# Performance work log

Hardware: AMD Instinct MI355X
Metric: run time of the kernel (lower is better)

Reference implementation:

```python
import jax, jax.numpy as jnp
import numpy as np
from jax.ops import segment_sum, segment_max

N, E = 50000, 800000
IN_FEATS, H, D_HID, N_CLASSES = 256, 4, 32, 47
NEG_SLOPE = 0.2


def leaky_relu(x, slope=NEG_SLOPE):
    return jnp.where(x >= 0, x, slope * x)


def gat_conv(h, W, attn_l, attn_r, src, dst, n_nodes, heads, d_out):
    # h: [N, F_in]; W: [F_in, heads*d_out]; attn_l/attn_r: [heads, d_out]
    feat = (h @ W).reshape(n_nodes, heads, d_out)          # [N, H, D]
    el = jnp.sum(feat * attn_l, axis=-1)                   # [N, H]
    er = jnp.sum(feat * attn_r, axis=-1)                   # [N, H]
    e = leaky_relu(el[src] + er[dst])                      # [E, H]
    # segment softmax over incoming edges of each dst node
    e_max = segment_max(e, dst, num_segments=n_nodes)      # [N, H]
    e_exp = jnp.exp(e - e_max[dst])                        # [E, H]
    denom = segment_sum(e_exp, dst, num_segments=n_nodes)  # [N, H]
    alpha = e_exp / denom[dst]                             # [E, H]
    msg = feat[src] * alpha[..., None]                     # [E, H, D]
    return segment_sum(msg, dst, num_segments=n_nodes)     # [N, H, D]


def setup_inputs() -> dict:
    key = jax.random.key(0)
    ks = jax.random.split(key, 12)
    hd = H * D_HID
    def glorot(k, shape):
        fan = shape[0] + shape[-1] if len(shape) == 2 else int(np.prod(shape))
        return jax.random.normal(k, shape, dtype=jnp.float32) * np.sqrt(2.0 / fan)
    return {
        "x": jax.random.normal(ks[0], (N, IN_FEATS), dtype=jnp.float32),
        "src": jax.random.randint(ks[1], (E,), 0, N),
        "dst": jax.random.randint(ks[2], (E,), 0, N),
        "W1": glorot(ks[3], (IN_FEATS, hd)),
        "al1": glorot(ks[4], (H, D_HID)),
        "ar1": glorot(ks[5], (H, D_HID)),
        "W2": glorot(ks[6], (hd, hd)),
        "al2": glorot(ks[7], (H, D_HID)),
        "ar2": glorot(ks[8], (H, D_HID)),
        "W3": glorot(ks[9], (hd, H * N_CLASSES)),
        "al3": glorot(ks[10], (H, N_CLASSES)),
        "ar3": glorot(ks[11], (H, N_CLASSES)),
    }


def reference(x, src, dst, W1, al1, ar1, W2, al2, ar2, W3, al3, ar3):
    # layer 1: ELU activation, flatten heads
    h = gat_conv(x, W1, al1, ar1, src, dst, N, H, D_HID)
    h = jax.nn.elu(h).reshape(N, H * D_HID)
    # layer 2
    h = gat_conv(h, W2, al2, ar2, src, dst, N, H, D_HID)
    h = jax.nn.elu(h).reshape(N, H * D_HID)
    # layer 3: no activation, mean over heads, log softmax
    h = gat_conv(h, W3, al3, ar3, src, dst, N, H, N_CLASSES)
    h = h.mean(axis=1)                                      # [N, n_classes]
    return jax.nn.log_softmax(h, axis=-1)
```

## Files before the change

kernel.cpp:

```cpp
#include <hip/hip_runtime.h>
#include <hip/hip_bf16.h>
#include <math.h>
#include <string.h>

#define N_NODES 50000
#define N_EDGES 800000
#define NH 4

typedef unsigned int u32;
typedef unsigned short u16;
typedef __attribute__((ext_vector_type(8))) short bf16x8;
typedef __attribute__((ext_vector_type(4))) float f32x4;

__device__ __forceinline__ u32 pack_bf2(float a, float b) {
    __hip_bfloat162 h2 = __float22bfloat162_rn(make_float2(a, b));
    u32 r;
    memcpy(&r, &h2, 4);
    return r;
}
__device__ __forceinline__ float2 bf2_to_f2(u32 u) {
    return make_float2(__uint_as_float(u << 16), __uint_as_float(u & 0xffff0000u));
}
__device__ __forceinline__ short bf16r(float f) {
    __hip_bfloat16 h = __float2bfloat16(f);
    short s;
    memcpy(&s, &h, 2);
    return s;
}

__device__ __forceinline__ float wred_max(float v) {
#pragma unroll
    for (int o = 32; o > 0; o >>= 1) v = fmaxf(v, __shfl_xor(v, o));
    return v;
}
__device__ __forceinline__ float wred_sum(float v) {
#pragma unroll
    for (int o = 32; o > 0; o >>= 1) v += __shfl_xor(v, o);
    return v;
}


__global__ void k_hist(const int* __restrict__ dst, int* __restrict__ deg) {
    int i = blockIdx.x * 256 + threadIdx.x;
    if (i < N_EDGES) atomicAdd(&deg[dst[i]], 1);
}

__global__ __launch_bounds__(1024) void k_scan1(const int* __restrict__ deg,
                                                int* __restrict__ offs,
                                                int* __restrict__ bsum) {
    __shared__ int tmp[1024];
    int b = blockIdx.x, t = threadIdx.x;
    int i = b * 1024 + t;
    int v = (i < N_NODES) ? deg[i] : 0;
    tmp[t] = v;
    __syncthreads();
    for (int off = 1; off < 1024; off <<= 1) {
        int add = (t >= off) ? tmp[t - off] : 0;
        __syncthreads();
        tmp[t] += add;
        __syncthreads();
    }
    if (i < N_NODES) offs[i] = tmp[t] - v;
    if (t == 1023) bsum[b] = tmp[t];
}

__global__ void k_scan2(int* __restrict__ bsum, int nb) {
    if (blockIdx.x == 0 && threadIdx.x == 0) {
        int run = 0;
        for (int b = 0; b < nb; ++b) { int v = bsum[b]; bsum[b] = run; run += v; }
    }
}

__global__ __launch_bounds__(1024) void k_scan3(int* __restrict__ offs,
                                                const int* __restrict__ bsum,
                                                int* __restrict__ cursor) {
    int b = blockIdx.x, t = threadIdx.x;
    int i = b * 1024 + t;
    if (i < N_NODES) {
        int o = offs[i] + bsum[b];
        offs[i] = o;
        cursor[i] = o;
    }
    if (b == 0 && t == 0) offs[N_NODES] = N_EDGES;
}

__global__ void k_scatter(const int* __restrict__ src, const int* __restrict__ dst,
                          int* __restrict__ cursor, int* __restrict__ csrc) {
    int i = blockIdx.x * 256 + threadIdx.x;
    if (i < N_EDGES) {
        int p = atomicAdd(&cursor[dst[i]], 1);
        csrc[p] = src[i];
    }
}

template <int K, int NOUT, int NP>
__global__ void prep_w(const float* __restrict__ W, u16* __restrict__ Wp) {
    constexpr int NT = NP / 16;
    int idx = blockIdx.x * 256 + threadIdx.x;
    int total = (K / 32) * NT * 64 * 8;
    if (idx >= total) return;
    int j = idx & 7;
    int lane = (idx >> 3) & 63;
    int rest = idx >> 9;
    int nt = rest % NT;
    int kt = rest / NT;
    int k = kt * 32 + (lane >> 4) * 8 + j;
    int col = nt * 16 + (lane & 15);
    float v = (col < NOUT) ? W[(size_t)k * NOUT + col] : 0.f;
    Wp[idx] = (u16)bf16r(v);
}

template <int K, int NOUT, int NP, bool AF32, bool DOTS>
__global__ __launch_bounds__(256) void gemm_mfma(const void* __restrict__ Av,
                                                 const u16* __restrict__ Wp,
                                                 u16* __restrict__ feat,
                                                 const float* __restrict__ al,
                                                 const float* __restrict__ ar,
                                                 float* __restrict__ el,
                                                 float* __restrict__ er) {
    constexpr int NT = NP / 16;
    constexpr int KT = K / 32;
    int w = threadIdx.x >> 6, l = threadIdx.x & 63;
    int tile_m0 = blockIdx.x * 64 + w * 16;
    int c15 = l & 15;
    int rowA = tile_m0 + c15;
    if (rowA >= N_NODES) rowA = N_NODES - 1;
    int g = l >> 4;

    f32x4 acc[NT];
#pragma unroll
    for (int nt = 0; nt < NT; ++nt) acc[nt] = (f32x4){0.f, 0.f, 0.f, 0.f};

    for (int kt = 0; kt < KT; ++kt) {
        bf16x8 a;
        if constexpr (AF32) {
            const float* ap = (const float*)Av + (size_t)rowA * K + kt * 32 + g * 8;
            float4 f0 = *reinterpret_cast<const float4*>(ap);
            float4 f1 = *reinterpret_cast<const float4*>(ap + 4);
            a[0] = bf16r(f0.x); a[1] = bf16r(f0.y); a[2] = bf16r(f0.z); a[3] = bf16r(f0.w);
            a[4] = bf16r(f1.x); a[5] = bf16r(f1.y); a[6] = bf16r(f1.z); a[7] = bf16r(f1.w);
        } else {
            a = *reinterpret_cast<const bf16x8*>((const u16*)Av + (size_t)rowA * K + kt * 32 + g * 8);
        }
        const u16* wp = Wp + ((size_t)kt * NT) * 512 + (size_t)l * 8;
#pragma unroll
        for (int nt = 0; nt < NT; ++nt) {
            bf16x8 b = *reinterpret_cast<const bf16x8*>(wp + nt * 512);
            acc[nt] = __builtin_amdgcn_mfma_f32_16x16x32_bf16(a, b, acc[nt], 0, 0, 0);
        }
    }

    int rowD0 = tile_m0 + g * 4;
#pragma unroll
    for (int nt = 0; nt < NT; ++nt) {
        int col = nt * 16 + c15;
#pragma unroll
        for (int r = 0; r < 4; ++r) {
            int row = rowD0 + r;
            if (row < N_NODES)
                feat[(size_t)row * NP + col] = (u16)bf16r(acc[nt][r]);
        }
    }

    if constexpr (DOTS) {
        float alv[NT], arv[NT];
#pragma unroll
        for (int nt = 0; nt < NT; ++nt) {
            alv[nt] = al[nt * 16 + c15];
            arv[nt] = ar[nt * 16 + c15];
        }
#pragma unroll
        for (int r = 0; r < 4; ++r) {
            float hlv[NH] = {0.f, 0.f, 0.f, 0.f};
            float hrv[NH] = {0.f, 0.f, 0.f, 0.f};
#pragma unroll
            for (int nt = 0; nt < NT; ++nt) {
                constexpr int NTH = NT / NH;
                int h = nt / NTH;
                hlv[h] = fmaf(acc[nt][r], alv[nt], hlv[h]);
                hrv[h] = fmaf(acc[nt][r], arv[nt], hrv[h]);
            }
#pragma unroll
            for (int o = 1; o < 16; o <<= 1) {
#pragma unroll
                for (int j = 0; j < NH; ++j) {
                    hlv[j] += __shfl_xor(hlv[j], o);
                    hrv[j] += __shfl_xor(hrv[j], o);
                }
            }
            int row = rowD0 + r;
            if (c15 == 0 && row < N_NODES) {
                *reinterpret_cast<float4*>(el + (size_t)row * NH) =
                    make_float4(hlv[0], hlv[1], hlv[2], hlv[3]);
                *reinterpret_cast<float4*>(er + (size_t)row * NH) =
                    make_float4(hrv[0], hrv[1], hrv[2], hrv[3]);
            }
        }
    }
}

template <int DH, int STRIDE>
__global__ __launch_bounds__(256) void attn_dots(const u16* __restrict__ feat,
                                                 const float* __restrict__ al,
                                                 const float* __restrict__ ar,
                                                 float* __restrict__ el,
                                                 float* __restrict__ er) {
    int wave = threadIdx.x >> 6, lane = threadIdx.x & 63;
    int n = blockIdx.x * 4 + wave;
    int h = lane >> 4, t = lane & 15;
    const u16* f = feat + (size_t)n * STRIDE + h * DH;
    const float* alh = al + h * DH;
    const float* arh = ar + h * DH;
    float sl = 0.f, sr = 0.f;
#pragma unroll
    for (int d0 = 0; d0 < DH; d0 += 16) {
        int d = d0 + t;
        if (d < DH) {
            float fv = __uint_as_float(((u32)f[d]) << 16);
            sl = fmaf(fv, alh[d], sl);
            sr = fmaf(fv, arh[d], sr);
        }
    }
#pragma unroll
    for (int o = 1; o < 16; o <<= 1) {
        sl += __shfl_xor(sl, o);
        sr += __shfl_xor(sr, o);
    }
    if (t == 0) { el[n * NH + h] = sl; er[n * NH + h] = sr; }
}

__device__ __forceinline__ int alpha_chunk(const float* __restrict__ el,
                                           const int* __restrict__ csrc,
                                           float4 erv, int base, int i1, int wave,
                                           float4 mref, float4 vinv, bool online,
                                           float (*lal)[64][4], int lane) {
    int e = base + lane;
    bool act = e < i1;
    int srcn = act ? csrc[e] : 0;
    float4 elv = make_float4(0.f, 0.f, 0.f, 0.f);
    if (act) elv = *reinterpret_cast<const float4*>(el + (size_t)srcn * NH);
    float e0 = elv.x + erv.x; e0 = e0 >= 0.f ? e0 : 0.2f * e0;
    float e1 = elv.y + erv.y; e1 = e1 >= 0.f ? e1 : 0.2f * e1;
    float e2 = elv.z + erv.z; e2 = e2 >= 0.f ? e2 : 0.2f * e2;
    float e3 = elv.w + erv.w; e3 = e3 >= 0.f ? e3 : 0.2f * e3;
    float4 a4;
    if (online) {
        const float NEG = -__builtin_inff();
        float f0 = act ? e0 : NEG, f1 = act ? e1 : NEG, f2 = act ? e2 : NEG, f3 = act ? e3 : NEG;
        float m0 = wred_max(f0), m1 = wred_max(f1), m2 = wred_max(f2), m3 = wred_max(f3);
        float p0 = act ? __expf(e0 - m0) : 0.f;
        float p1 = act ? __expf(e1 - m1) : 0.f;
        float p2 = act ? __expf(e2 - m2) : 0.f;
        float p3 = act ? __expf(e3 - m3) : 0.f;
        float s0 = wred_sum(p0), s1 = wred_sum(p1), s2 = wred_sum(p2), s3 = wred_sum(p3);
        a4 = make_float4(act ? p0 / s0 : 0.f, act ? p1 / s1 : 0.f,
                         act ? p2 / s2 : 0.f, act ? p3 / s3 : 0.f);
    } else {
        a4 = make_float4(act ? __expf(e0 - mref.x) * vinv.x : 0.f,
                         act ? __expf(e1 - mref.y) * vinv.y : 0.f,
                         act ? __expf(e2 - mref.z) * vinv.z : 0.f,
                         act ? __expf(e3 - mref.w) * vinv.w : 0.f);
    }
    *reinterpret_cast<float4*>(&lal[wave][lane][0]) = a4;
    return srcn;
}

__device__ __forceinline__ void stats_pass(const float* __restrict__ el,
                                           const int* __restrict__ csrc,
                                           float4 erv, int i0, int i1, int lane,
                                           float4& mout, float4& vout) {
    const float NEG = -__builtin_inff();
    float m0 = NEG, m1 = NEG, m2 = NEG, m3 = NEG;
    float s0 = 0.f, s1 = 0.f, s2 = 0.f, s3 = 0.f;
    for (int base = i0; base < i1; base += 64) {
        int i = base + lane;
        bool act = i < i1;
        int srcn = act ? csrc[i] : 0;
        float4 elv = make_float4(0.f, 0.f, 0.f, 0.f);
        if (act) elv = *reinterpret_cast<const float4*>(el + (size_t)srcn * NH);
        float e0 = elv.x + erv.x; e0 = e0 >= 0.f ? e0 : 0.2f * e0;
        float e1 = elv.y + erv.y; e1 = e1 >= 0.f ? e1 : 0.2f * e1;
        float e2 = elv.z + erv.z; e2 = e2 >= 0.f ? e2 : 0.2f * e2;
        float e3 = elv.w + erv.w; e3 = e3 >= 0.f ? e3 : 0.2f * e3;
        if (!act) { e0 = NEG; e1 = NEG; e2 = NEG; e3 = NEG; }
        float c0 = wred_max(e0), c1 = wred_max(e1), c2 = wred_max(e2), c3 = wred_max(e3);
        float nm0 = fmaxf(m0, c0), nm1 = fmaxf(m1, c1), nm2 = fmaxf(m2, c2), nm3 = fmaxf(m3, c3);
        float p0 = act ? __expf(e0 - nm0) : 0.f;
        float p1 = act ? __expf(e1 - nm1) : 0.f;
        float p2 = act ? __expf(e2 - nm2) : 0.f;
        float p3 = act ? __expf(e3 - nm3) : 0.f;
        float S0 = wred_sum(p0), S1 = wred_sum(p1), S2 = wred_sum(p2), S3 = wred_sum(p3);
        s0 = s0 * __expf(m0 - nm0) + S0; m0 = nm0;
        s1 = s1 * __expf(m1 - nm1) + S1; m1 = nm1;
        s2 = s2 * __expf(m2 - nm2) + S2; m2 = nm2;
        s3 = s3 * __expf(m3 - nm3) + S3; m3 = nm3;
    }
    mout = make_float4(m0, m1, m2, m3);
    vout = make_float4(1.f / s0, 1.f / s1, 1.f / s2, 1.f / s3);
}

__global__ __launch_bounds__(256) void gat_agg128(const u16* __restrict__ feat,
                                                  const float* __restrict__ el,
                                                  const float* __restrict__ er,
                                                  const int* __restrict__ offs,
                                                  const int* __restrict__ csrc,
                                                  u16* __restrict__ out) {
    __shared__ float lal[4][64][4];
    int wave = threadIdx.x >> 6;
    int lane = threadIdx.x & 63;
    int n = blockIdx.x * 4 + wave;
    int h = lane >> 4;
    int i0 = offs[n], i1 = offs[n + 1];
    int d = i1 - i0;
    float ax = 0.f, ay = 0.f;
    if (d > 0) {
        float4 erv = *reinterpret_cast<const float4*>(er + (size_t)n * NH);
        float4 mref = make_float4(0.f, 0.f, 0.f, 0.f), vinv = mref;
        bool onechunk = d <= 64;
        if (!onechunk) stats_pass(el, csrc, erv, i0, i1, lane, mref, vinv);
        for (int base = i0; base < i1; base += 64) {
            int srcn = alpha_chunk(el, csrc, erv, base, i1, wave, mref, vinv, onechunk, lal, lane);
            int cnt = i1 - base; if (cnt > 64) cnt = 64;
            int cpad = (cnt + 3) & ~3;
            for (int j = 0; j < cpad; j += 4) {
                int s0 = __shfl(srcn, j + 0);
                int s1 = __shfl(srcn, j + 1);
                int s2 = __shfl(srcn, j + 2);
                int s3 = __shfl(srcn, j + 3);
                float a0 = lal[wave][j + 0][h];
                float a1 = lal[wave][j + 1][h];
                float a2 = lal[wave][j + 2][h];
                float a3 = lal[wave][j + 3][h];
                u32 q0 = *reinterpret_cast<const u32*>(feat + (size_t)s0 * 128 + 2 * lane);
                u32 q1 = *reinterpret_cast<const u32*>(feat + (size_t)s1 * 128 + 2 * lane);
                u32 q2 = *reinterpret_cast<const u32*>(feat + (size_t)s2 * 128 + 2 * lane);
                u32 q3 = *reinterpret_cast<const u32*>(feat + (size_t)s3 * 128 + 2 * lane);
                float2 v;
                v = bf2_to_f2(q0); ax = fmaf(a0, v.x, ax); ay = fmaf(a0, v.y, ay);
                v = bf2_to_f2(q1); ax = fmaf(a1, v.x, ax); ay = fmaf(a1, v.y, ay);
                v = bf2_to_f2(q2); ax = fmaf(a2, v.x, ax); ay = fmaf(a2, v.y, ay);
                v = bf2_to_f2(q3); ax = fmaf(a3, v.x, ax); ay = fmaf(a3, v.y, ay);
            }
        }
    }
    float ox = ax > 0.f ? ax : expm1f(ax);
    float oy = ay > 0.f ? ay : expm1f(ay);
    *reinterpret_cast<u32*>(out + (size_t)n * 128 + 2 * lane) = pack_bf2(ox, oy);
}

__global__ __launch_bounds__(256) void gat_agg_final(const u16* __restrict__ feat,
                                                     const float* __restrict__ el,
                                                     const float* __restrict__ er,
                                                     const int* __restrict__ offs,
                                                     const int* __restrict__ csrc,
                                                     float* __restrict__ out) {
    __shared__ float lal[4][64][4];
    __shared__ float lds[4][188];
    int wave = threadIdx.x >> 6;
    int lane = threadIdx.x & 63;
    int n = blockIdx.x * 4 + wave;
    int e0 = 2 * lane;
    int h00 = e0 / 47;
    int h01 = (e0 + 1) / 47;
    bool act30 = lane < 30;
    int h10 = act30 ? (128 + e0) / 47 : 2;
    int h11 = act30 ? (129 + e0) / 47 : 2;
    int i0 = offs[n], i1 = offs[n + 1];
    int d = i1 - i0;
    float a00 = 0.f, a01 = 0.f, a10 = 0.f, a11 = 0.f;
    if (d > 0) {
        float4 erv = *reinterpret_cast<const float4*>(er + (size_t)n * NH);
        float4 mref = make_float4(0.f, 0.f, 0.f, 0.f), vinv = mref;
        bool onechunk = d <= 64;
        if (!onechunk) stats_pass(el, csrc, erv, i0, i1, lane, mref, vinv);
        for (int base = i0; base < i1; base += 64) {
            int srcn = alpha_chunk(el, csrc, erv, base, i1, wave, mref, vinv, onechunk, lal, lane);
            int cnt = i1 - base; if (cnt > 64) cnt = 64;
            int cpad = (cnt + 1) & ~1;
            for (int j = 0; j < cpad; j += 2) {
                int sA = __shfl(srcn, j + 0);
                int sB = __shfl(srcn, j + 1);
                float wA00 = lal[wave][j + 0][h00], wA01 = lal[wave][j + 0][h01];
                float wA10 = lal[wave][j + 0][h10], wA11 = lal[wave][j + 0][h11];
                float wB00 = lal[wave][j + 1][h00], wB01 = lal[wave][j + 1][h01];
                float wB10 = lal[wave][j + 1][h10], wB11 = lal[wave][j + 1][h11];
                const u16* rA = feat + (size_t)sA * 192;
                const u16* rB = feat + (size_t)sB * 192;
                u32 uA0 = *reinterpret_cast<const u32*>(rA + e0);
                u32 uB0 = *reinterpret_cast<const u32*>(rB + e0);
                u32 uA1 = act30 ? *reinterpret_cast<const u32*>(rA + 128 + e0) : 0u;
                u32 uB1 = act30 ? *reinterpret_cast<const u32*>(rB + 128 + e0) : 0u;
                float2 v;
                v = bf2_to_f2(uA0); a00 = fmaf(wA00, v.x, a00); a01 = fmaf(wA01, v.y, a01);
                v = bf2_to_f2(uA1); a10 = fmaf(wA10, v.x, a10); a11 = fmaf(wA11, v.y, a11);
                v = bf2_to_f2(uB0); a00 = fmaf(wB00, v.x, a00); a01 = fmaf(wB01, v.y, a01);
                v = bf2_to_f2(uB1); a10 = fmaf(wB10, v.x, a10); a11 = fmaf(wB11, v.y, a11);
            }
        }
    }
    lds[wave][e0] = a00;
    lds[wave][e0 + 1] = a01;
    if (act30) {
        lds[wave][128 + e0] = a10;
        lds[wave][129 + e0] = a11;
    }
    __syncthreads();
    float u = (lane < 47)
                  ? 0.25f * (lds[wave][lane] + lds[wave][47 + lane] +
                             lds[wave][94 + lane] + lds[wave][141 + lane])
                  : -__builtin_inff();
    float mx = u;
#pragma unroll
    for (int o = 32; o > 0; o >>= 1) mx = fmaxf(mx, __shfl_xor(mx, o));
    float ex = (lane < 47) ? __expf(u - mx) : 0.f;
    float sm = ex;
#pragma unroll
    for (int o = 32; o > 0; o >>= 1) sm += __shfl_xor(sm, o);
    if (lane < 47) out[(size_t)n * 47 + lane] = u - mx - logf(sm);
}


extern "C" void kernel_launch(void* const* d_in, const int* in_sizes, int n_in,
                              void* d_out, int out_size, void* d_ws, size_t ws_size,
                              hipStream_t stream) {
    const float* x = (const float*)d_in[0];
    const int* src = (const int*)d_in[1];
    const int* dst = (const int*)d_in[2];
    const float* W1 = (const float*)d_in[3];
    const float* al1 = (const float*)d_in[4];
    const float* ar1 = (const float*)d_in[5];
    const float* W2 = (const float*)d_in[6];
    const float* al2 = (const float*)d_in[7];
    const float* ar2 = (const float*)d_in[8];
    const float* W3 = (const float*)d_in[9];
    const float* al3 = (const float*)d_in[10];
    const float* ar3 = (const float*)d_in[11];
    float* out = (float*)d_out;

    char* p = (char*)d_ws;
    auto alloc = [&](size_t bytes) {
        char* r = p;
        p += (bytes + 255) & ~(size_t)255;
        return r;
    };
    u16* bufA = (u16*)alloc((size_t)N_NODES * 128 * 2);
    u16* bufC = (u16*)alloc((size_t)N_NODES * 128 * 2);
    u16* featb = (u16*)alloc((size_t)N_NODES * 192 * 2);
    float* el = (float*)alloc((size_t)N_NODES * NH * 4);
    float* er = (float*)alloc((size_t)N_NODES * NH * 4);
    u16* wp1 = (u16*)alloc((size_t)(256 / 32) * 8 * 512 * 2);
    u16* wp2 = (u16*)alloc((size_t)(128 / 32) * 8 * 512 * 2);
    u16* wp3 = (u16*)alloc((size_t)(128 / 32) * 12 * 512 * 2);
    int* deg = (int*)alloc((size_t)N_NODES * 4);
    int* offs = (int*)alloc((size_t)(N_NODES + 1) * 4);
    int* cursor = (int*)alloc((size_t)N_NODES * 4);
    int* bsum = (int*)alloc(64 * 4);
    int* csrc = (int*)alloc((size_t)N_EDGES * 4);

    prep_w<256, 128, 128><<<(8 * 8 * 512 + 255) / 256, 256, 0, stream>>>(W1, wp1);
    prep_w<128, 128, 128><<<(4 * 8 * 512 + 255) / 256, 256, 0, stream>>>(W2, wp2);
    prep_w<128, 188, 192><<<(4 * 12 * 512 + 255) / 256, 256, 0, stream>>>(W3, wp3);

    hipMemsetAsync(deg, 0, (size_t)N_NODES * 4, stream);
    k_hist<<<(N_EDGES + 255) / 256, 256, 0, stream>>>(dst, deg);
    k_scan1<<<49, 1024, 0, stream>>>(deg, offs, bsum);
    k_scan2<<<1, 64, 0, stream>>>(bsum, 49);
    k_scan3<<<49, 1024, 0, stream>>>(offs, bsum, cursor);
    k_scatter<<<(N_EDGES + 255) / 256, 256, 0, stream>>>(src, dst, cursor, csrc);

    int gemm_grid = (N_NODES + 63) / 64;
    gemm_mfma<256, 128, 128, true, true><<<gemm_grid, 256, 0, stream>>>(x, wp1, featb, al1, ar1, el, er);
    gat_agg128<<<N_NODES / 4, 256, 0, stream>>>(featb, el, er, offs, csrc, bufA);
    gemm_mfma<128, 128, 128, false, true><<<gemm_grid, 256, 0, stream>>>(bufA, wp2, featb, al2, ar2, el, er);
    gat_agg128<<<N_NODES / 4, 256, 0, stream>>>(featb, el, er, offs, csrc, bufC);
    gemm_mfma<128, 188, 192, false, false><<<gemm_grid, 256, 0, stream>>>(bufC, wp3, featb, nullptr, nullptr, nullptr, nullptr);
    attn_dots<47, 192><<<N_NODES / 4, 256, 0, stream>>>(featb, al3, ar3, el, er);
    gat_agg_final<<<N_NODES / 4, 256, 0, stream>>>(featb, el, er, offs, csrc, out);
}
```

Baseline: 336.0 us.

## Pad layer-3 heads to 48 columns, fuse attention dots into GEMM, transpose alpha LDS

Layer-3 weights are repacked so each head occupies 48 padded columns. This lets the GEMM epilogue compute el/er directly, and the separate attn_dots kernel is removed. The aggregation kernels now store alpha head-major plus source indices in LDS. That replaces per-edge shuffles and scalar LDS reads with vector LDS loads, and the final kernel processes four edges per iteration. The cost is extra padded columns and larger LDS use per block.

```diff
diff --git a/kernel.cpp b/kernel.cpp
--- a/kernel.cpp
+++ b/kernel.cpp
@@ -110,7 +110,25 @@
     Wp[idx] = (u16)bf16r(v);
 }
 
-template <int K, int NOUT, int NP, bool AF32, bool DOTS>
+template <int K>
+__global__ void prep_w3(const float* __restrict__ W, u16* __restrict__ Wp) {
+    constexpr int NT = 12;
+    int idx = blockIdx.x * 256 + threadIdx.x;
+    int total = (K / 32) * NT * 64 * 8;
+    if (idx >= total) return;
+    int j = idx & 7;
+    int lane = (idx >> 3) & 63;
+    int rest = idx >> 9;
+    int nt = rest % NT;
+    int kt = rest / NT;
+    int k = kt * 32 + (lane >> 4) * 8 + j;
+    int col = nt * 16 + (lane & 15);
+    int h = col / 48, d = col % 48;
+    float v = (d < 47) ? W[(size_t)k * 188 + h * 47 + d] : 0.f;
+    Wp[idx] = (u16)bf16r(v);
+}
+
+template <int K, int NOUT, int NP, bool AF32, bool DOTS, bool HEADPAD>
 __global__ __launch_bounds__(256) void gemm_mfma(const void* __restrict__ Av,
                                                  const u16* __restrict__ Wp,
                                                  u16* __restrict__ feat,
@@ -166,8 +184,19 @@
         float alv[NT], arv[NT];
 #pragma unroll
         for (int nt = 0; nt < NT; ++nt) {
-            alv[nt] = al[nt * 16 + c15];
-            arv[nt] = ar[nt * 16 + c15];
+            if constexpr (HEADPAD) {
+                int h = nt / 3, m = nt % 3;
+                if (m == 2) {
+                    alv[nt] = (c15 < 15) ? al[h * 47 + 32 + c15] : 0.f;
+                    arv[nt] = (c15 < 15) ? ar[h * 47 + 32 + c15] : 0.f;
+                } else {
+                    alv[nt] = al[h * 47 + m * 16 + c15];
+                    arv[nt] = ar[h * 47 + m * 16 + c15];
+                }
+            } else {
+                alv[nt] = al[nt * 16 + c15];
+                arv[nt] = ar[nt * 16 + c15];
+            }
         }
 #pragma unroll
         for (int r = 0; r < 4; ++r) {
@@ -199,41 +228,12 @@
     }
 }
 
-template <int DH, int STRIDE>
-__global__ __launch_bounds__(256) void attn_dots(const u16* __restrict__ feat,
-                                                 const float* __restrict__ al,
-                                                 const float* __restrict__ ar,
-                                                 float* __restrict__ el,
-                                                 float* __restrict__ er) {
-    int wave = threadIdx.x >> 6, lane = threadIdx.x & 63;
-    int n = blockIdx.x * 4 + wave;
-    int h = lane >> 4, t = lane & 15;
-    const u16* f = feat + (size_t)n * STRIDE + h * DH;
-    const float* alh = al + h * DH;
-    const float* arh = ar + h * DH;
-    float sl = 0.f, sr = 0.f;
-#pragma unroll
-    for (int d0 = 0; d0 < DH; d0 += 16) {
-        int d = d0 + t;
-        if (d < DH) {
-            float fv = __uint_as_float(((u32)f[d]) << 16);
-            sl = fmaf(fv, alh[d], sl);
-            sr = fmaf(fv, arh[d], sr);
-        }
-    }
-#pragma unroll
-    for (int o = 1; o < 16; o <<= 1) {
-        sl += __shfl_xor(sl, o);
-        sr += __shfl_xor(sr, o);
-    }
-    if (t == 0) { el[n * NH + h] = sl; er[n * NH + h] = sr; }
-}
-
-__device__ __forceinline__ int alpha_chunk(const float* __restrict__ el,
-                                           const int* __restrict__ csrc,
-                                           float4 erv, int base, int i1, int wave,
-                                           float4 mref, float4 vinv, bool online,
-                                           float (*lal)[64][4], int lane) {
+__device__ __forceinline__ void alpha_chunk_T(const float* __restrict__ el,
+                                              const int* __restrict__ csrc,
+                                              float4 erv, int base, int i1,
+                                              float4 mref, float4 vinv, bool online,
+                                              float* __restrict__ lalT,
+                                              int* __restrict__ lsrc, int lane) {
     int e = base + lane;
     bool act = e < i1;
     int srcn = act ? csrc[e] : 0;
@@ -261,8 +261,11 @@
                          act ? __expf(e2 - mref.z) * vinv.z : 0.f,
                          act ? __expf(e3 - mref.w) * vinv.w : 0.f);
     }
-    *reinterpret_cast<float4*>(&lal[wave][lane][0]) = a4;
-    return srcn;
+    lalT[0 * 64 + lane] = a4.x;
+    lalT[1 * 64 + lane] = a4.y;
+    lalT[2 * 64 + lane] = a4.z;
+    lalT[3 * 64 + lane] = a4.w;
+    lsrc[lane] = srcn;
 }
 
 __device__ __forceinline__ void stats_pass(const float* __restrict__ el,
@@ -305,7 +308,8 @@
                                                   const int* __restrict__ offs,
                                                   const int* __restrict__ csrc,
                                                   u16* __restrict__ out) {
-    __shared__ float lal[4][64][4];
+    __shared__ float lalT[4][4][64];
+    __shared__ int lsrc[4][64];
     int wave = threadIdx.x >> 6;
     int lane = threadIdx.x & 63;
     int n = blockIdx.x * 4 + wave;
@@ -319,27 +323,22 @@
         bool onechunk = d <= 64;
         if (!onechunk) stats_pass(el, csrc, erv, i0, i1, lane, mref, vinv);
         for (int base = i0; base < i1; base += 64) {
-            int srcn = alpha_chunk(el, csrc, erv, base, i1, wave, mref, vinv, onechunk, lal, lane);
+            alpha_chunk_T(el, csrc, erv, base, i1, mref, vinv, onechunk,
+                          &lalT[wave][0][0], &lsrc[wave][0], lane);
             int cnt = i1 - base; if (cnt > 64) cnt = 64;
             int cpad = (cnt + 3) & ~3;
             for (int j = 0; j < cpad; j += 4) {
-                int s0 = __shfl(srcn, j + 0);
-                int s1 = __shfl(srcn, j + 1);
-                int s2 = __shfl(srcn, j + 2);
-                int s3 = __shfl(srcn, j + 3);
-                float a0 = lal[wave][j + 0][h];
-                float a1 = lal[wave][j + 1][h];
-                float a2 = lal[wave][j + 2][h];
-                float a3 = lal[wave][j + 3][h];
-                u32 q0 = *reinterpret_cast<const u32*>(feat + (size_t)s0 * 128 + 2 * lane);
-                u32 q1 = *reinterpret_cast<const u32*>(feat + (size_t)s1 * 128 + 2 * lane);
-                u32 q2 = *reinterpret_cast<const u32*>(feat + (size_t)s2 * 128 + 2 * lane);
-                u32 q3 = *reinterpret_cast<const u32*>(feat + (size_t)s3 * 128 + 2 * lane);
+                int4 sv = *reinterpret_cast<const int4*>(&lsrc[wave][j]);
+                float4 aq = *reinterpret_cast<const float4*>(&lalT[wave][h][j]);
+                u32 q0 = *reinterpret_cast<const u32*>(feat + (size_t)sv.x * 128 + 2 * lane);
+                u32 q1 = *reinterpret_cast<const u32*>(feat + (size_t)sv.y * 128 + 2 * lane);
+                u32 q2 = *reinterpret_cast<const u32*>(feat + (size_t)sv.z * 128 + 2 * lane);
+                u32 q3 = *reinterpret_cast<const u32*>(feat + (size_t)sv.w * 128 + 2 * lane);
                 float2 v;
-                v = bf2_to_f2(q0); ax = fmaf(a0, v.x, ax); ay = fmaf(a0, v.y, ay);
-                v = bf2_to_f2(q1); ax = fmaf(a1, v.x, ax); ay = fmaf(a1, v.y, ay);
-                v = bf2_to_f2(q2); ax = fmaf(a2, v.x, ax); ay = fmaf(a2, v.y, ay);
-                v = bf2_to_f2(q3); ax = fmaf(a3, v.x, ax); ay = fmaf(a3, v.y, ay);
+                v = bf2_to_f2(q0); ax = fmaf(aq.x, v.x, ax); ay = fmaf(aq.x, v.y, ay);
+                v = bf2_to_f2(q1); ax = fmaf(aq.y, v.x, ax); ay = fmaf(aq.y, v.y, ay);
+                v = bf2_to_f2(q2); ax = fmaf(aq.z, v.x, ax); ay = fmaf(aq.z, v.y, ay);
+                v = bf2_to_f2(q3); ax = fmaf(aq.w, v.x, ax); ay = fmaf(aq.w, v.y, ay);
             }
         }
     }
@@ -354,17 +353,16 @@
                                                      const int* __restrict__ offs,
                                                      const int* __restrict__ csrc,
                                                      float* __restrict__ out) {
-    __shared__ float lal[4][64][4];
-    __shared__ float lds[4][188];
+    __shared__ float lalT[4][4][64];
+    __shared__ int lsrc[4][64];
+    __shared__ float lds[4][192];
     int wave = threadIdx.x >> 6;
     int lane = threadIdx.x & 63;
     int n = blockIdx.x * 4 + wave;
     int e0 = 2 * lane;
-    int h00 = e0 / 47;
-    int h01 = (e0 + 1) / 47;
-    bool act30 = lane < 30;
-    int h10 = act30 ? (128 + e0) / 47 : 2;
-    int h11 = act30 ? (129 + e0) / 47 : 2;
+    bool up = lane < 32;
+    int hLo = e0 / 48;
+    int hHi = up ? (128 + e0) / 48 : 3;
     int i0 = offs[n], i1 = offs[n + 1];
     int d = i1 - i0;
     float a00 = 0.f, a01 = 0.f, a10 = 0.f, a11 = 0.f;
@@ -374,40 +372,48 @@
         bool onechunk = d <= 64;
         if (!onechunk) stats_pass(el, csrc, erv, i0, i1, lane, mref, vinv);
         for (int base = i0; base < i1; base += 64) {
-            int srcn = alpha_chunk(el, csrc, erv, base, i1, wave, mref, vinv, onechunk, lal, lane);
+            alpha_chunk_T(el, csrc, erv, base, i1, mref, vinv, onechunk,
+                          &lalT[wave][0][0], &lsrc[wave][0], lane);
             int cnt = i1 - base; if (cnt > 64) cnt = 64;
-            int cpad = (cnt + 1) & ~1;
-            for (int j = 0; j < cpad; j += 2) {
-                int sA = __shfl(srcn, j + 0);
-                int sB = __shfl(srcn, j + 1);
-                float wA00 = lal[wave][j + 0][h00], wA01 = lal[wave][j + 0][h01];
-                float wA10 = lal[wave][j + 0][h10], wA11 = lal[wave][j + 0][h11];
-                float wB00 = lal[wave][j + 1][h00], wB01 = lal[wave][j + 1][h01];
-                float wB10 = lal[wave][j + 1][h10], wB11 = lal[wave][j + 1][h11];
-                const u16* rA = feat + (size_t)sA * 192;
-                const u16* rB = feat + (size_t)sB * 192;
-                u32 uA0 = *reinterpret_cast<const u32*>(rA + e0);
-                u32 uB0 = *reinterpret_cast<const u32*>(rB + e0);
-                u32 uA1 = act30 ? *reinterpret_cast<const u32*>(rA + 128 + e0) : 0u;
-                u32 uB1 = act30 ? *reinterpret_cast<const u32*>(rB + 128 + e0) : 0u;
+            int cpad = (cnt + 3) & ~3;
+            for (int j = 0; j < cpad; j += 4) {
+                int4 sv = *reinterpret_cast<const int4*>(&lsrc[wave][j]);
+                float4 wlo = *reinterpret_cast<const float4*>(&lalT[wave][hLo][j]);
+                float4 whi = *reinterpret_cast<const float4*>(&lalT[wave][hHi][j]);
+                const u16* rA = feat + (size_t)sv.x * 192;
+                const u16* rB = feat + (size_t)sv.y * 192;
+                const u16* rC = feat + (size_t)sv.z * 192;
+                const u16* rD = feat + (size_t)sv.w * 192;
+                u32 a0 = *reinterpret_cast<const u32*>(rA + e0);
+                u32 b0 = *reinterpret_cast<const u32*>(rB + e0);
+                u32 c0 = *reinterpret_cast<const u32*>(rC + e0);
+                u32 d0 = *reinterpret_cast<const u32*>(rD + e0);
+                u32 a1 = up ? *reinterpret_cast<const u32*>(rA + 128 + e0) : 0u;
+                u32 b1 = up ? *reinterpret_cast<const u32*>(rB + 128 + e0) : 0u;
+                u32 c1 = up ? *reinterpret_cast<const u32*>(rC + 128 + e0) : 0u;
+                u32 d1 = up ? *reinterpret_cast<const u32*>(rD + 128 + e0) : 0u;
                 float2 v;
-                v = bf2_to_f2(uA0); a00 = fmaf(wA00, v.x, a00); a01 = fmaf(wA01, v.y, a01);
-                v = bf2_to_f2(uA1); a10 = fmaf(wA10, v.x, a10); a11 = fmaf(wA11, v.y, a11);
-                v = bf2_to_f2(uB0); a00 = fmaf(wB00, v.x, a00); a01 = fmaf(wB01, v.y, a01);
-                v = bf2_to_f2(uB1); a10 = fmaf(wB10, v.x, a10); a11 = fmaf(wB11, v.y, a11);
+                v = bf2_to_f2(a0); a00 = fmaf(wlo.x, v.x, a00); a01 = fmaf(wlo.x, v.y, a01);
+                v = bf2_to_f2(b0); a00 = fmaf(wlo.y, v.x, a00); a01 = fmaf(wlo.y, v.y, a01);
+                v = bf2_to_f2(c0); a00 = fmaf(wlo.z, v.x, a00); a01 = fmaf(wlo.z, v.y, a01);
+                v = bf2_to_f2(d0); a00 = fmaf(wlo.w, v.x, a00); a01 = fmaf(wlo.w, v.y, a01);
+                v = bf2_to_f2(a1); a10 = fmaf(whi.x, v.x, a10); a11 = fmaf(whi.x, v.y, a11);
+                v = bf2_to_f2(b1); a10 = fmaf(whi.y, v.x, a10); a11 = fmaf(whi.y, v.y, a11);
+                v = bf2_to_f2(c1); a10 = fmaf(whi.z, v.x, a10); a11 = fmaf(whi.z, v.y, a11);
+                v = bf2_to_f2(d1); a10 = fmaf(whi.w, v.x, a10); a11 = fmaf(whi.w, v.y, a11);
             }
         }
     }
     lds[wave][e0] = a00;
     lds[wave][e0 + 1] = a01;
-    if (act30) {
+    if (up) {
         lds[wave][128 + e0] = a10;
         lds[wave][129 + e0] = a11;
     }
     __syncthreads();
     float u = (lane < 47)
-                  ? 0.25f * (lds[wave][lane] + lds[wave][47 + lane] +
-                             lds[wave][94 + lane] + lds[wave][141 + lane])
+                  ? 0.25f * (lds[wave][lane] + lds[wave][48 + lane] +
+                             lds[wave][96 + lane] + lds[wave][144 + lane])
                   : -__builtin_inff();
     float mx = u;
 #pragma unroll
@@ -459,7 +465,7 @@
 
     prep_w<256, 128, 128><<<(8 * 8 * 512 + 255) / 256, 256, 0, stream>>>(W1, wp1);
     prep_w<128, 128, 128><<<(4 * 8 * 512 + 255) / 256, 256, 0, stream>>>(W2, wp2);
-    prep_w<128, 188, 192><<<(4 * 12 * 512 + 255) / 256, 256, 0, stream>>>(W3, wp3);
+    prep_w3<128><<<(4 * 12 * 512 + 255) / 256, 256, 0, stream>>>(W3, wp3);
 
     hipMemsetAsync(deg, 0, (size_t)N_NODES * 4, stream);
     k_hist<<<(N_EDGES + 255) / 256, 256, 0, stream>>>(dst, deg);
@@ -469,11 +475,10 @@
     k_scatter<<<(N_EDGES + 255) / 256, 256, 0, stream>>>(src, dst, cursor, csrc);
 
     int gemm_grid = (N_NODES + 63) / 64;
-    gemm_mfma<256, 128, 128, true, true><<<gemm_grid, 256, 0, stream>>>(x, wp1, featb, al1, ar1, el, er);
+    gemm_mfma<256, 128, 128, true, true, false><<<gemm_grid, 256, 0, stream>>>(x, wp1, featb, al1, ar1, el, er);
     gat_agg128<<<N_NODES / 4, 256, 0, stream>>>(featb, el, er, offs, csrc, bufA);
-    gemm_mfma<128, 128, 128, false, true><<<gemm_grid, 256, 0, stream>>>(bufA, wp2, featb, al2, ar2, el, er);
+    gemm_mfma<128, 128, 128, false, true, false><<<gemm_grid, 256, 0, stream>>>(bufA, wp2, featb, al2, ar2, el, er);
     gat_agg128<<<N_NODES / 4, 256, 0, stream>>>(featb, el, er, offs, csrc, bufC);
-    gemm_mfma<128, 188, 192, false, false><<<gemm_grid, 256, 0, stream>>>(bufC, wp3, featb, nullptr, nullptr, nullptr, nullptr);
-    attn_dots<47, 192><<<N_NODES / 4, 256, 0, stream>>>(featb, al3, ar3, el, er);
+    gemm_mfma<128, 192, 192, false, true, true><<<gemm_grid, 256, 0, stream>>>(bufC, wp3, featb, al3, ar3, el, er);
     gat_agg_final<<<N_NODES / 4, 256, 0, stream>>>(featb, el, er, offs, csrc, out);
 }
```

Measured after the change: 314.1 us. 6.5% less time.
